# Performance work log

Hardware: AMD Instinct MI355X
Metric: run time of the kernel (lower is better)

## Reference

```python
import jax, jax.numpy as jnp
import numpy as np

B, S, D, H, HD = 2, 2048, 1024, 16, 64


def setup_inputs() -> dict:
    key = jax.random.key(0)
    ks = jax.random.split(key, 11)
    scale_in = 1.0 / np.sqrt(D)
    return {
        "query": jax.random.normal(ks[0], (B, S, D), jnp.float32),
        "key": jax.random.normal(ks[1], (B, S, D), jnp.float32),
        "value": jax.random.normal(ks[2], (B, S, D), jnp.float32),
        "Wq": jax.random.normal(ks[3], (H, D, HD), jnp.float32) * scale_in,
        "bq": jax.random.normal(ks[4], (H, HD), jnp.float32) * 0.02,
        "Wk": jax.random.normal(ks[5], (H, D, HD), jnp.float32) * scale_in,
        "bk": jax.random.normal(ks[6], (H, HD), jnp.float32) * 0.02,
        "Wv": jax.random.normal(ks[7], (H, D, HD), jnp.float32) * scale_in,
        "bv": jax.random.normal(ks[8], (H, HD), jnp.float32) * 0.02,
        "Wo": jax.random.normal(ks[9], (D, D), jnp.float32) * scale_in,
        "bo": jax.random.normal(ks[10], (D,), jnp.float32) * 0.02,
    }


def reference(query, key, value, Wq, bq, Wk, bk, Wv, bv, Wo, bo):
    # Per-head projections, batched over heads (equivalent to the ModuleList loop).
    q = jnp.einsum('bsd,hdk->bhsk', query, Wq) + bq[None, :, None, :]   # [B,H,S,HD]
    k = jnp.einsum('bsd,hdk->bhsk', key, Wk) + bk[None, :, None, :]
    v = jnp.einsum('bsd,hdk->bhsk', value, Wv) + bv[None, :, None, :]
    scale = 1.0 / jnp.sqrt(jnp.asarray(q.shape[-1], q.dtype))
    scores = jnp.einsum('bhsk,bhtk->bhst', q, k) * scale                # [B,H,S,S]
    attn = jax.nn.softmax(scores, axis=-1)
    ctx = jnp.einsum('bhst,bhtk->bhsk', attn, v)                        # [B,H,S,HD]
    # Concat heads along last dim: [B,S,H*HD] == [B,S,D]
    x = jnp.transpose(ctx, (0, 2, 1, 3)).reshape(ctx.shape[0], ctx.shape[2], -1)
    return x @ Wo + bo
```

## Files before the change

### kernel.cpp

```cpp
#include <hip/hip_runtime.h>
#include <hip/hip_bf16.h>

typedef __bf16 bf16;
typedef __bf16 bf16x8 __attribute__((ext_vector_type(8)));
typedef __bf16 bf16x4 __attribute__((ext_vector_type(4)));
typedef __bf16 bf16x2 __attribute__((ext_vector_type(2)));
typedef float floatx4 __attribute__((ext_vector_type(4)));
typedef float floatx16 __attribute__((ext_vector_type(16)));
typedef int intx4 __attribute__((ext_vector_type(4)));

#define B_SZ 2
#define S_LEN 2048
#define D_DIM 1024
#define H_CNT 16
#define HD_DIM 64
#define M_ROWS 4096
#define QSCALE 0.18033688011112042f

__device__ __forceinline__ void async_ld16(const bf16* g, bf16* s) {
    __builtin_amdgcn_global_load_lds((const __attribute__((address_space(1))) void*)g,
                                     (__attribute__((address_space(3))) void*)s, 16, 0, 0);
}

__device__ __forceinline__ floatx4 mfma16(bf16x8 a, bf16x8 b, floatx4 c) {
    return __builtin_amdgcn_mfma_f32_16x16x32_bf16(a, b, c, 0, 0, 0);
}
__device__ __forceinline__ floatx16 mfma32(bf16x8 a, bf16x8 b, floatx16 c) {
    return __builtin_amdgcn_mfma_f32_32x32x16_bf16(a, b, c, 0, 0, 0);
}

__device__ __forceinline__ bf16x8 mkfrag(int a0, int a1, int b0, int b1) {
    asm("v_permlane32_swap_b32 %0, %1" : "+v"(a0), "+v"(b0));
    asm("v_permlane32_swap_b32 %0, %1" : "+v"(a1), "+v"(b1));
    intx4 q = {a0, a1, b0, b1};
    return __builtin_bit_cast(bf16x8, q);
}

struct PrepArgs {
    const float* cast_src[3]; bf16* cast_dst[3];
    const float* w_src[3];    bf16* w_dst[3];
    const float* wo;          bf16* wo_t;
};
__global__ __launch_bounds__(256) void prep(PrepArgs a) {
    __shared__ bf16 tile[32][33];
    const int bx = blockIdx.x, tid = threadIdx.x;
    if (bx < 12288) {
        const int t = bx >> 12, blk = bx & 4095;
        const float* s = a.cast_src[t];
        bf16* d = a.cast_dst[t];
        size_t i = ((size_t)blk * 256 + tid) * 4;
        float4 v = *(const float4*)(s + i);
        bf16x4 o = { (bf16)v.x, (bf16)v.y, (bf16)v.z, (bf16)v.w };
        *(bf16x4*)(d + i) = o;
        return;
    }
    int tx = tid & 31, ty = tid >> 5;
    const float* src; bf16* dst; int r0, c0, C, R;
    if (bx < 15360) {
        int idx = bx - 12288;
        int z = idx >> 6, xy = idx & 63;
        int mat = z >> 4, head = z & 15;
        src = a.w_src[mat] + (size_t)head * D_DIM * HD_DIM;
        dst = a.w_dst[mat] + (size_t)head * D_DIM * HD_DIM;
        r0 = (xy & 31) * 32; c0 = (xy >> 5) * 32; C = HD_DIM; R = D_DIM;
    } else {
        int idx = bx - 15360;
        src = a.wo; dst = a.wo_t;
        r0 = (idx & 31) * 32; c0 = (idx >> 5) * 32; C = D_DIM; R = D_DIM;
    }
#pragma unroll
    for (int i = 0; i < 32; i += 8)
        tile[ty + i][tx] = (bf16)src[(size_t)(r0 + ty + i) * C + c0 + tx];
    __syncthreads();
#pragma unroll
    for (int i = 0; i < 32; i += 8)
        dst[(size_t)(c0 + ty + i) * R + r0 + tx] = tile[tx][ty + i];
}

__global__ __launch_bounds__(256) void transpose2d(const bf16* __restrict__ src,
                                                   bf16* __restrict__ dst, int R, int C) {
    __shared__ bf16 tile[32][33];
    size_t zoff = (size_t)blockIdx.z * R * C;
    src += zoff; dst += zoff;
    int r0 = blockIdx.x * 32, c0 = blockIdx.y * 32;
    int tx = threadIdx.x & 31, ty = threadIdx.x >> 5;
#pragma unroll
    for (int i = 0; i < 32; i += 8) tile[ty + i][tx] = src[(size_t)(r0 + ty + i) * C + c0 + tx];
    __syncthreads();
#pragma unroll
    for (int i = 0; i < 32; i += 8) dst[(size_t)(c0 + ty + i) * R + r0 + tx] = tile[tx][ty + i];
}

struct GemmPtrs { const bf16* A; const bf16* BT; const float* bias; bf16* C; float* Cf; float scale; };
struct GemmArgs { GemmPtrs p[3]; int mode; };

__global__ __launch_bounds__(256) void gemm_bt(GemmArgs args) {
    __shared__ __align__(16) bf16 As[128 * 32];
    __shared__ __align__(16) bf16 Bs[128 * 32];
    const GemmPtrs P = args.p[blockIdx.z];
    const int tid = threadIdx.x, wave = tid >> 6, lane = tid & 63;
    const int quad = lane >> 4, l15 = lane & 15;
    const int bm = blockIdx.x * 128, bn = blockIdx.y * 128;
    const int wm = (wave >> 1) * 64, wn = (wave & 1) * 64;

    floatx4 acc[4][4];
#pragma unroll
    for (int i = 0; i < 4; i++)
#pragma unroll
        for (int j = 0; j < 4; j++) acc[i][j] = (floatx4){0.f, 0.f, 0.f, 0.f};

    const int srow = (lane >> 2);
    const int scol = (((lane & 3) ^ ((srow >> 1) & 3)) << 3);
    const int ck = ((quad ^ ((l15 >> 1) & 3)) << 3);
    for (int k0 = 0; k0 < 1024; k0 += 32) {
#pragma unroll
        for (int it = 0; it < 2; ++it) {
            int issue = it * 4 + wave;
            int row = issue * 16 + srow;
            async_ld16(P.A + (size_t)(bm + row) * 1024 + k0 + scol, &As[issue * 512]);
            async_ld16(P.BT + (size_t)(bn + row) * 1024 + k0 + scol, &Bs[issue * 512]);
        }
        __syncthreads();
        bf16x8 af[4], bfr[4];
#pragma unroll
        for (int mi = 0; mi < 4; mi++)
            af[mi] = *(const bf16x8*)&As[(wm + mi * 16 + l15) * 32 + ck];
#pragma unroll
        for (int ni = 0; ni < 4; ni++)
            bfr[ni] = *(const bf16x8*)&Bs[(wn + ni * 16 + l15) * 32 + ck];
#pragma unroll
        for (int mi = 0; mi < 4; mi++)
#pragma unroll
            for (int ni = 0; ni < 4; ni++) acc[mi][ni] = mfma16(af[mi], bfr[ni], acc[mi][ni]);
        __syncthreads();
    }
#pragma unroll
    for (int ni = 0; ni < 4; ni++) {
        int col = bn + wn + ni * 16 + l15;
        float bb = P.bias[col];
#pragma unroll
        for (int mi = 0; mi < 4; mi++) {
#pragma unroll
            for (int r = 0; r < 4; r++) {
                int row = bm + wm + mi * 16 + quad * 4 + r;
                float v = (acc[mi][ni][r] + bb) * P.scale;
                if (args.mode == 0) {
                    P.Cf[(size_t)row * 1024 + col] = v;
                } else {
                    int b = row >> 11, s2 = row & 2047, h = col >> 6, hd = col & 63;
                    P.C[(((size_t)(b * H_CNT + h)) * S_LEN + s2) * HD_DIM + hd] = (bf16)v;
                }
            }
        }
    }
}

__global__ __launch_bounds__(256) void attn(const bf16* __restrict__ Qg, const bf16* __restrict__ Kg,
                                            const bf16* __restrict__ Vtg, bf16* __restrict__ ctx) {
    __shared__ __align__(16) bf16 Ks[2][8192];
    __shared__ __align__(16) bf16 Vs[2][8192];
    const int tid = threadIdx.x, wave = tid >> 6, lane = tid & 63;
    const int l31 = lane & 31, half = lane >> 5;
    const int bid = blockIdx.x;
    const int bh = (bid >> 1) & 31;
    const int qb = ((bid >> 6) << 1) | (bid & 1);
    const int q0blk = qb * 128;
    const bf16* Kp = Kg + (size_t)bh * S_LEN * HD_DIM;
    const bf16* Vp = Vtg + (size_t)bh * HD_DIM * S_LEN;

#pragma unroll
    for (int it = 0; it < 4; ++it) {
        int i = it * 4 + wave;
        int f = i * 512 + lane * 8;
        int sub = f >> 12, rem = f & 4095;
        int c = rem >> 9, r = (rem >> 3) & 63;
        async_ld16(Kp + (size_t)(sub * 64 + r) * HD_DIM + c * 8, &Ks[0][i * 512]);
        async_ld16(Vp + (size_t)r * S_LEN + sub * 64 + c * 8, &Vs[0][i * 512]);
    }
    bf16x8 qf[4];
    {
        const bf16* qrow = Qg + ((size_t)bh * S_LEN + q0blk + wave * 32 + l31) * HD_DIM;
#pragma unroll
        for (int kb = 0; kb < 4; ++kb)
            qf[kb] = *(const bf16x8*)(qrow + (2 * kb + half) * 8);
    }
    __syncthreads();

    float l_i = 0.f;
    floatx16 o0 = {0}, o1 = {0};

    for (int rd = 0; rd < 16; ++rd) {
        const int cur = rd & 1;
        if (rd < 15) {
            int t0n = (rd + 1) * 128;
#pragma unroll
            for (int it = 0; it < 4; ++it) {
                int i = it * 4 + wave;
                int f = i * 512 + lane * 8;
                int sub = f >> 12, rem = f & 4095;
                int c = rem >> 9, r = (rem >> 3) & 63;
                async_ld16(Kp + (size_t)(t0n + sub * 64 + r) * HD_DIM + c * 8, &Ks[cur ^ 1][i * 512]);
                async_ld16(Vp + (size_t)r * S_LEN + t0n + sub * 64 + c * 8, &Vs[cur ^ 1][i * 512]);
            }
        }
#pragma unroll
        for (int sub = 0; sub < 2; ++sub) {
            const bf16* Kt = &Ks[cur][sub * 4096];
            const bf16* Vt = &Vs[cur][sub * 4096];
            floatx16 sc0 = {0}, sc1 = {0};
            __builtin_amdgcn_s_setprio(1);
#pragma unroll
            for (int kb = 0; kb < 4; ++kb) {
                bf16x8 k0 = *(const bf16x8*)&Kt[(2 * kb + half) * 512 + l31 * 8];
                bf16x8 k1 = *(const bf16x8*)&Kt[(2 * kb + half) * 512 + (32 + l31) * 8];
                sc0 = mfma32(k0, qf[kb], sc0);
                sc1 = mfma32(k1, qf[kb], sc1);
            }
            __builtin_amdgcn_s_setprio(0);
            float rs = 0.f;
            int w0[8], w1[8];
#pragma unroll
            for (int e = 0; e < 16; e += 2) {
                float p0 = __builtin_amdgcn_exp2f(sc0[e]);
                float p1 = __builtin_amdgcn_exp2f(sc0[e + 1]);
                rs += p0 + p1;
                bf16x2 t2 = {(bf16)p0, (bf16)p1};
                w0[e >> 1] = __builtin_bit_cast(int, t2);
            }
#pragma unroll
            for (int e = 0; e < 16; e += 2) {
                float p0 = __builtin_amdgcn_exp2f(sc1[e]);
                float p1 = __builtin_amdgcn_exp2f(sc1[e + 1]);
                rs += p0 + p1;
                bf16x2 t2 = {(bf16)p0, (bf16)p1};
                w1[e >> 1] = __builtin_bit_cast(int, t2);
            }
            l_i += rs;
            bf16x8 pfr[4];
            pfr[0] = mkfrag(w0[0], w0[1], w0[2], w0[3]);
            pfr[1] = mkfrag(w0[4], w0[5], w0[6], w0[7]);
            pfr[2] = mkfrag(w1[0], w1[1], w1[2], w1[3]);
            pfr[3] = mkfrag(w1[4], w1[5], w1[6], w1[7]);
            __builtin_amdgcn_s_setprio(1);
#pragma unroll
            for (int kb = 0; kb < 4; ++kb) {
                bf16x8 v0 = *(const bf16x8*)&Vt[(2 * kb + half) * 512 + l31 * 8];
                bf16x8 v1 = *(const bf16x8*)&Vt[(2 * kb + half) * 512 + (32 + l31) * 8];
                o0 = mfma32(v0, pfr[kb], o0);
                o1 = mfma32(v1, pfr[kb], o1);
            }
            __builtin_amdgcn_s_setprio(0);
        }
        __syncthreads();
    }
    l_i += __shfl_xor(l_i, 32);
    int b = bh >> 4, hh = bh & 15;
    float inv = 1.f / l_i;
    bf16* Sw = &Ks[0][0] + wave * 1280;
#pragma unroll
    for (int s2 = 0; s2 < 2; ++s2) {
        const floatx16 oo = s2 ? o1 : o0;
#pragma unroll
        for (int e = 0; e < 16; ++e) {
            int hd = (e & 3) + 8 * (e >> 2) + 4 * half;
            Sw[l31 * 40 + hd] = (bf16)(oo[e] * inv);
        }
#pragma unroll
        for (int p = 0; p < 2; ++p) {
            int q = p * 16 + (lane >> 2), part = lane & 3;
            bf16x8 v = *(const bf16x8*)&Sw[q * 40 + part * 8];
            int s = q0blk + wave * 32 + q;
            *(bf16x8*)&ctx[((size_t)(b * S_LEN + s)) * D_DIM + hh * 64 + s2 * 32 + part * 8] = v;
        }
    }
}

extern "C" void kernel_launch(void* const* d_in, const int* in_sizes, int n_in,
                              void* d_out, int out_size, void* d_ws, size_t ws_size,
                              hipStream_t stream) {
    const float* query = (const float*)d_in[0];
    const float* key   = (const float*)d_in[1];
    const float* value = (const float*)d_in[2];
    const float* Wq = (const float*)d_in[3];
    const float* bq = (const float*)d_in[4];
    const float* Wk = (const float*)d_in[5];
    const float* bk = (const float*)d_in[6];
    const float* Wv = (const float*)d_in[7];
    const float* bv = (const float*)d_in[8];
    const float* Wo = (const float*)d_in[9];
    const float* bo = (const float*)d_in[10];
    float* out = (float*)d_out;

    bf16* ws = (bf16*)d_ws;
    const size_t ASZ = (size_t)M_ROWS * D_DIM;
    const size_t WSZ = (size_t)H_CNT * D_DIM * HD_DIM;
    const size_t TSZ = (size_t)B_SZ * H_CNT * S_LEN * HD_DIM;
    bf16* Qc  = ws;
    bf16* Kc  = Qc + ASZ;
    bf16* Vc  = Kc + ASZ;
    bf16* WqT = Vc + ASZ;
    bf16* WkT = WqT + WSZ;
    bf16* WvT = WkT + WSZ;
    bf16* WoT = WvT + WSZ;
    bf16* Qb  = WoT + (size_t)D_DIM * D_DIM;
    bf16* Kb  = Qb + TSZ;
    bf16* Vb  = Kb + TSZ;
    bf16* Vtb = Vb + TSZ;
    bf16* ctx = Vtb + TSZ;

    dim3 blk(256);

    PrepArgs pa;
    pa.cast_src[0] = query; pa.cast_src[1] = key; pa.cast_src[2] = value;
    pa.cast_dst[0] = Qc;    pa.cast_dst[1] = Kc;  pa.cast_dst[2] = Vc;
    pa.w_src[0] = Wq; pa.w_src[1] = Wk; pa.w_src[2] = Wv;
    pa.w_dst[0] = WqT; pa.w_dst[1] = WkT; pa.w_dst[2] = WvT;
    pa.wo = Wo; pa.wo_t = WoT;
    prep<<<dim3(16384), blk, 0, stream>>>(pa);

    GemmArgs qkv;
    qkv.p[0] = {Qc, WqT, bq, Qb, nullptr, QSCALE};
    qkv.p[1] = {Kc, WkT, bk, Kb, nullptr, 1.0f};
    qkv.p[2] = {Vc, WvT, bv, Vb, nullptr, 1.0f};
    qkv.mode = 1;
    gemm_bt<<<dim3(32, 8, 3), blk, 0, stream>>>(qkv);

    transpose2d<<<dim3(64, 2, 32), blk, 0, stream>>>(Vb, Vtb, 2048, 64);

    attn<<<dim3(512), blk, 0, stream>>>(Qb, Kb, Vtb, ctx);

    GemmArgs og;
    og.p[0] = {ctx, WoT, bo, nullptr, out, 1.0f};
    og.p[1] = og.p[0]; og.p[2] = og.p[0];
    og.mode = 0;
    gemm_bt<<<dim3(32, 8, 1), blk, 0, stream>>>(og);
}
```

Before: 247.3 us.

## Triple-buffer attention K/V tiles with finer-grained vmcnt waits and barriers

The attention kernel moves from double-buffered 128-key K/V tiles to triple-buffered 64-key tiles. Each step now uses an explicit s_waitcnt vmcnt plus a raw s_barrier, so two tiles stay in flight while the current one is computed, instead of a full __syncthreads after each 128-key block. Global addresses are precomputed once and bumped by pointer increments, and LDS use drops from 64KB to 48KB, which may allow more resident blocks per CU. The trade-off is more frequent, though lighter, barriers and a hand-tuned wait count that must stay in step with the number of issued loads.

```diff
diff --git a/kernel.cpp b/kernel.cpp
--- a/kernel.cpp
+++ b/kernel.cpp
@@ -35,6 +35,8 @@
     intx4 q = {a0, a1, b0, b1};
     return __builtin_bit_cast(bf16x8, q);
 }
+
+#define VMWAIT(N) asm volatile("s_waitcnt vmcnt(" #N ")" ::: "memory")
 
 struct PrepArgs {
     const float* cast_src[3]; bf16* cast_dst[3];
@@ -157,8 +159,8 @@
 
 __global__ __launch_bounds__(256) void attn(const bf16* __restrict__ Qg, const bf16* __restrict__ Kg,
                                             const bf16* __restrict__ Vtg, bf16* __restrict__ ctx) {
-    __shared__ __align__(16) bf16 Ks[2][8192];
-    __shared__ __align__(16) bf16 Vs[2][8192];
+    __shared__ __align__(16) bf16 Ks[3][4096];
+    __shared__ __align__(16) bf16 Vs[3][4096];
     const int tid = threadIdx.x, wave = tid >> 6, lane = tid & 63;
     const int l31 = lane & 31, half = lane >> 5;
     const int bid = blockIdx.x;
@@ -168,15 +170,25 @@
     const bf16* Kp = Kg + (size_t)bh * S_LEN * HD_DIM;
     const bf16* Vp = Vtg + (size_t)bh * HD_DIM * S_LEN;
 
-#pragma unroll
-    for (int it = 0; it < 4; ++it) {
-        int i = it * 4 + wave;
-        int f = i * 512 + lane * 8;
-        int sub = f >> 12, rem = f & 4095;
-        int c = rem >> 9, r = (rem >> 3) & 63;
-        async_ld16(Kp + (size_t)(sub * 64 + r) * HD_DIM + c * 8, &Ks[0][i * 512]);
-        async_ld16(Vp + (size_t)r * S_LEN + sub * 64 + c * 8, &Vs[0][i * 512]);
-    }
+    const int i0 = wave, i1 = 4 + wave;
+    const int f0 = i0 * 512 + lane * 8, f1 = i1 * 512 + lane * 8;
+    const int c0i = f0 >> 9, r0i = (f0 >> 3) & 63;
+    const int c1i = f1 >> 9, r1i = (f1 >> 3) & 63;
+    const bf16* kg0 = Kp + (size_t)r0i * HD_DIM + c0i * 8;
+    const bf16* kg1 = Kp + (size_t)r1i * HD_DIM + c1i * 8;
+    const bf16* vg0 = Vp + (size_t)r0i * S_LEN + c0i * 8;
+    const bf16* vg1 = Vp + (size_t)r1i * S_LEN + c1i * 8;
+
+#define STAGE(BUF) do { \
+        async_ld16(kg0, &Ks[BUF][i0 * 512]); \
+        async_ld16(kg1, &Ks[BUF][i1 * 512]); \
+        async_ld16(vg0, &Vs[BUF][i0 * 512]); \
+        async_ld16(vg1, &Vs[BUF][i1 * 512]); \
+        kg0 += 64 * HD_DIM; kg1 += 64 * HD_DIM; vg0 += 64; vg1 += 64; \
+    } while (0)
+
+    STAGE(0);
+    STAGE(1);
     bf16x8 qf[4];
     {
         const bf16* qrow = Qg + ((size_t)bh * S_LEN + q0blk + wave * 32 + l31) * HD_DIM;
@@ -189,71 +201,68 @@
     float l_i = 0.f;
     floatx16 o0 = {0}, o1 = {0};
 
-    for (int rd = 0; rd < 16; ++rd) {
-        const int cur = rd & 1;
-        if (rd < 15) {
-            int t0n = (rd + 1) * 128;
-#pragma unroll
-            for (int it = 0; it < 4; ++it) {
-                int i = it * 4 + wave;
-                int f = i * 512 + lane * 8;
-                int sub = f >> 12, rem = f & 4095;
-                int c = rem >> 9, r = (rem >> 3) & 63;
-                async_ld16(Kp + (size_t)(t0n + sub * 64 + r) * HD_DIM + c * 8, &Ks[cur ^ 1][i * 512]);
-                async_ld16(Vp + (size_t)r * S_LEN + t0n + sub * 64 + c * 8, &Vs[cur ^ 1][i * 512]);
-            }
-        }
-#pragma unroll
-        for (int sub = 0; sub < 2; ++sub) {
-            const bf16* Kt = &Ks[cur][sub * 4096];
-            const bf16* Vt = &Vs[cur][sub * 4096];
-            floatx16 sc0 = {0}, sc1 = {0};
-            __builtin_amdgcn_s_setprio(1);
-#pragma unroll
-            for (int kb = 0; kb < 4; ++kb) {
-                bf16x8 k0 = *(const bf16x8*)&Kt[(2 * kb + half) * 512 + l31 * 8];
-                bf16x8 k1 = *(const bf16x8*)&Kt[(2 * kb + half) * 512 + (32 + l31) * 8];
-                sc0 = mfma32(k0, qf[kb], sc0);
-                sc1 = mfma32(k1, qf[kb], sc1);
-            }
-            __builtin_amdgcn_s_setprio(0);
-            float rs = 0.f;
-            int w0[8], w1[8];
-#pragma unroll
-            for (int e = 0; e < 16; e += 2) {
-                float p0 = __builtin_amdgcn_exp2f(sc0[e]);
-                float p1 = __builtin_amdgcn_exp2f(sc0[e + 1]);
-                rs += p0 + p1;
-                bf16x2 t2 = {(bf16)p0, (bf16)p1};
-                w0[e >> 1] = __builtin_bit_cast(int, t2);
-            }
-#pragma unroll
-            for (int e = 0; e < 16; e += 2) {
-                float p0 = __builtin_amdgcn_exp2f(sc1[e]);
-                float p1 = __builtin_amdgcn_exp2f(sc1[e + 1]);
-                rs += p0 + p1;
-                bf16x2 t2 = {(bf16)p0, (bf16)p1};
-                w1[e >> 1] = __builtin_bit_cast(int, t2);
-            }
-            l_i += rs;
-            bf16x8 pfr[4];
-            pfr[0] = mkfrag(w0[0], w0[1], w0[2], w0[3]);
-            pfr[1] = mkfrag(w0[4], w0[5], w0[6], w0[7]);
-            pfr[2] = mkfrag(w1[0], w1[1], w1[2], w1[3]);
-            pfr[3] = mkfrag(w1[4], w1[5], w1[6], w1[7]);
-            __builtin_amdgcn_s_setprio(1);
-#pragma unroll
-            for (int kb = 0; kb < 4; ++kb) {
-                bf16x8 v0 = *(const bf16x8*)&Vt[(2 * kb + half) * 512 + l31 * 8];
-                bf16x8 v1 = *(const bf16x8*)&Vt[(2 * kb + half) * 512 + (32 + l31) * 8];
-                o0 = mfma32(v0, pfr[kb], o0);
-                o1 = mfma32(v1, pfr[kb], o1);
-            }
-            __builtin_amdgcn_s_setprio(0);
-        }
-        __syncthreads();
-    }
+    auto compute = [&](const bf16* Kt, const bf16* Vt) {
+        floatx16 sc0 = {0}, sc1 = {0};
+        __builtin_amdgcn_s_setprio(1);
+#pragma unroll
+        for (int kb = 0; kb < 4; ++kb) {
+            bf16x8 k0 = *(const bf16x8*)&Kt[(2 * kb + half) * 512 + l31 * 8];
+            bf16x8 k1 = *(const bf16x8*)&Kt[(2 * kb + half) * 512 + (32 + l31) * 8];
+            sc0 = mfma32(k0, qf[kb], sc0);
+            sc1 = mfma32(k1, qf[kb], sc1);
+        }
+        __builtin_amdgcn_s_setprio(0);
+        float rs = 0.f;
+        int w0[8], w1[8];
+#pragma unroll
+        for (int e = 0; e < 16; e += 2) {
+            float p0 = __builtin_amdgcn_exp2f(sc0[e]);
+            float p1 = __builtin_amdgcn_exp2f(sc0[e + 1]);
+            rs += p0 + p1;
+            bf16x2 t2 = {(bf16)p0, (bf16)p1};
+            w0[e >> 1] = __builtin_bit_cast(int, t2);
+        }
+#pragma unroll
+        for (int e = 0; e < 16; e += 2) {
+            float p0 = __builtin_amdgcn_exp2f(sc1[e]);
+            float p1 = __builtin_amdgcn_exp2f(sc1[e + 1]);
+            rs += p0 + p1;
+            bf16x2 t2 = {(bf16)p0, (bf16)p1};
+            w1[e >> 1] = __builtin_bit_cast(int, t2);
+        }
+        l_i += rs;
+        bf16x8 pfr[4];
+        pfr[0] = mkfrag(w0[0], w0[1], w0[2], w0[3]);
+        pfr[1] = mkfrag(w0[4], w0[5], w0[6], w0[7]);
+        pfr[2] = mkfrag(w1[0], w1[1], w1[2], w1[3]);
+        pfr[3] = mkfrag(w1[4], w1[5], w1[6], w1[7]);
+        __builtin_amdgcn_s_setprio(1);
+#pragma unroll
+        for (int kb = 0; kb < 4; ++kb) {
+            bf16x8 v0 = *(const bf16x8*)&Vt[(2 * kb + half) * 512 + l31 * 8];
+            bf16x8 v1 = *(const bf16x8*)&Vt[(2 * kb + half) * 512 + (32 + l31) * 8];
+            o0 = mfma32(v0, pfr[kb], o0);
+            o1 = mfma32(v1, pfr[kb], o1);
+        }
+        __builtin_amdgcn_s_setprio(0);
+    };
+
+    for (int it3 = 0; it3 < 10; ++it3) {
+        VMWAIT(4); __builtin_amdgcn_s_barrier();
+        STAGE(2);  compute(&Ks[0][0], &Vs[0][0]);
+        VMWAIT(4); __builtin_amdgcn_s_barrier();
+        STAGE(0);  compute(&Ks[1][0], &Vs[1][0]);
+        VMWAIT(4); __builtin_amdgcn_s_barrier();
+        STAGE(1);  compute(&Ks[2][0], &Vs[2][0]);
+    }
+    VMWAIT(4); __builtin_amdgcn_s_barrier();
+    compute(&Ks[0][0], &Vs[0][0]);
+    VMWAIT(0); __builtin_amdgcn_s_barrier();
+    compute(&Ks[1][0], &Vs[1][0]);
+#undef STAGE
+
     l_i += __shfl_xor(l_i, 32);
+    __syncthreads();
     int b = bh >> 4, hh = bh & 15;
     float inv = 1.f / l_i;
     bf16* Sw = &Ks[0][0] + wave * 1280;
```

New measurement: 252.5 us. 1.02x slower.
